# Kernel tuning notes

Measured on AMD Instinct MI355X. Metric: run time of the kernel, lower is better.

## Reference

```python
import jax, jax.numpy as jnp
import numpy as np

G = 32; N = G * G          # gridsize, num_nodes per graph
A = 16                      # n_agents
B = 32                      # batch_size
E = 4096                    # edges per graph (~4-neighbor grid)
F_IN = 16                   # input_dim
H = 64                      # hidden_dim
L = 3                       # n_graph_layers
MID = F_IN + L * H          # 208
CAT = 2 * MID + H           # 480
MIN_VAL = -1e8


def _layer_norm(x, g, b, eps=1e-5):
    m = x.mean(-1, keepdims=True)
    v = x.var(-1, keepdims=True)
    return (x - m) * jax.lax.rsqrt(v + eps) * g + b


def setup_inputs() -> dict:
    key = jax.random.key(0)
    ks = jax.random.split(key, 16)
    inp = {}
    inp["graph_nodes"] = jax.random.normal(ks[0], (B, N, F_IN), jnp.float32)
    inp["graph_edge_links"] = jax.random.randint(ks[1], (B, 2, E), 0, N)
    inp["agent_locations"] = jax.random.randint(ks[2], (B, A), 0, N)
    inp["mask"] = jax.random.bernoulli(ks[3], 0.5, (B, A * N))
    inp["dist_matrix"] = jax.random.uniform(ks[4], (N, N), jnp.float32)
    dims = [F_IN] + [H] * L
    k = 5
    for l in range(L):
        inp[f"conv{l}_W"] = jax.random.normal(ks[k], (dims[l], H), jnp.float32) * 0.05
        inp[f"conv{l}_b"] = jnp.zeros((H,), jnp.float32)
        inp[f"conv{l}_g"] = jnp.ones((H,), jnp.float32)
        inp[f"conv{l}_beta"] = jnp.zeros((H,), jnp.float32)
        k += 1
    inp["edges_W"] = jax.random.normal(ks[k], (1, H), jnp.float32) * 0.05
    inp["edges_b"] = jnp.zeros((H,), jnp.float32)
    inp["actor1_W"] = jax.random.normal(ks[k + 1], (CAT, MID), jnp.float32) * 0.05
    inp["actor1_b"] = jnp.zeros((MID,), jnp.float32)
    inp["bn_g"] = jnp.ones((MID,), jnp.float32)
    inp["bn_b"] = jnp.zeros((MID,), jnp.float32)
    inp["actor2_W"] = jax.random.normal(ks[k + 2], (MID, 1), jnp.float32) * 0.05
    inp["actor2_b"] = jnp.zeros((1,), jnp.float32)
    return inp


def reference(graph_nodes, graph_edge_links, agent_locations, mask, dist_matrix,
              conv0_W, conv0_b, conv0_g, conv0_beta,
              conv1_W, conv1_b, conv1_g, conv1_beta,
              conv2_W, conv2_b, conv2_g, conv2_beta,
              edges_W, edges_b, actor1_W, actor1_b, bn_g, bn_b,
              actor2_W, actor2_b):
    # --- batch graphs: offset node indices per graph (Batch.from_data_list) ---
    x = graph_nodes.reshape(B * N, F_IN)
    offs = (jnp.arange(B) * N)[:, None, None]
    ei = (graph_edge_links + offs).transpose(1, 0, 2).reshape(2, B * E)
    src, dst = ei[0], ei[1]

    conv_params = [(conv0_W, conv0_b, conv0_g, conv0_beta),
                   (conv1_W, conv1_b, conv1_g, conv1_beta),
                   (conv2_W, conv2_b, conv2_g, conv2_beta)]
    outs = [x]
    for W, bb, g, beta in conv_params:
        # GINConv with eps=-1: (1+eps)*x_i == 0, so out = mlp(sum_j x_j)
        agg = jax.ops.segment_sum(x[src], dst, num_segments=B * N)
        x = jax.nn.relu(_layer_norm(agg @ W + bb, g, beta))  # mlp relu; outer .relu() idempotent
        outs.append(x)
    xc = jnp.concatenate(outs, axis=1).reshape(B, N, MID)

    # --- all-pairs (agent, node) feature build ---
    a = jnp.take_along_axis(xc, agent_locations[:, :, None], axis=1)  # [B, A, MID]
    a = jnp.repeat(a, N, axis=1)                                      # [B, A*N, MID]
    bfeat = jnp.tile(xc, (1, A, 1))                                   # [B, A*N, MID]
    c = dist_matrix[agent_locations].reshape(B, A * N, 1)             # [B, A*N, 1]
    c = c @ edges_W + edges_b                                         # [B, A*N, H]
    h = jnp.concatenate([a, bfeat, c], axis=2).reshape(-1, CAT)

    h = h @ actor1_W + actor1_b
    mu = h.mean(0)
    var = h.var(0)
    h = (h - mu) * jax.lax.rsqrt(var + 1e-5) * bn_g + bn_b  # BatchNorm1d, training stats
    h = jax.nn.relu(h)
    logits = (h @ actor2_W + actor2_b).reshape(B, A * N)
    logits = jnp.where(mask, logits, MIN_VAL)
    return jax.nn.softmax(logits, axis=1)
```

## Files before the change

kernel.cpp:

```cpp
#include <hip/hip_runtime.h>
#include <cstddef>

#define B_    32
#define N_    1024
#define E_    4096
#define A_    16
#define FIN_  16
#define H_    64
#define MID_  208
#define NODES (B_ * N_)
#define NEDGE (B_ * E_)
#define ROWS  (B_ * A_ * N_)
#define AN_   (A_ * N_)

__device__ __forceinline__ float readlane_f(float v, int l) {
  return __uint_as_float(__builtin_amdgcn_readlane(__float_as_uint(v), l));
}

__global__ __launch_bounds__(256) void k_front(const int* __restrict__ el,
                                               const float* __restrict__ dist,
                                               const int* __restrict__ loc,
                                               const float* __restrict__ W1,
                                               const float* __restrict__ eW,
                                               const float* __restrict__ eb,
                                               const float* __restrict__ b1,
                                               int* __restrict__ rowptr,
                                               int* __restrict__ counts,
                                               int* __restrict__ ssrc,
                                               float* __restrict__ d1row,
                                               float* __restrict__ c2row,
                                               float* __restrict__ e1,
                                               float* __restrict__ cu,
                                               float* __restrict__ base) {
  __shared__ int cnt[1024];
  __shared__ int cur[1024];
  __shared__ int part[256];
  __shared__ int loc_s[16];
  int blk = blockIdx.x, t = threadIdx.x;
  if (blk < 32) {
    int b = blk;
    for (int i = t; i < 1024; i += 256) cnt[i] = 0;
    __syncthreads();
    const int* srcp = el + b * (2 * E_);
    const int* dstp = srcp + E_;
    for (int i = t; i < E_; i += 256) atomicAdd(&cnt[dstp[i]], 1);
    __syncthreads();
    int4 c4 = *(const int4*)&cnt[t * 4];
    int s = c4.x + c4.y + c4.z + c4.w;
    part[t] = s;
    __syncthreads();
    for (int off = 1; off < 256; off <<= 1) {
      int v = (t >= off) ? part[t - off] : 0;
      __syncthreads();
      part[t] += v;
      __syncthreads();
    }
    int prev = ((t == 0) ? 0 : part[t - 1]) + b * E_;
    int p0 = prev, p1 = p0 + c4.x, p2 = p1 + c4.y, p3 = p2 + c4.z;
    *(int4*)&rowptr[b * 1024 + t * 4] = make_int4(p0, p1, p2, p3);
    *(int4*)&counts[b * 1024 + t * 4] = c4;
    cur[t * 4 + 0] = p0;
    cur[t * 4 + 1] = p1;
    cur[t * 4 + 2] = p2;
    cur[t * 4 + 3] = p3;
    __syncthreads();
    for (int i = t; i < E_; i += 256) {
      int dl = dstp[i];
      int sl = srcp[i];
      int pos = atomicAdd(&cur[dl], 1);
      ssrc[pos] = b * N_ + sl;
    }
  } else if (blk < 288) {
    int lane = t & 63, w = t >> 6;
    int r = (blk - 32) * 4 + w;
    const float* dr = dist + (size_t)r * N_;
    float s = 0.f, c2 = 0.f;
#pragma unroll
    for (int k = 0; k < 16; k++) {
      float v = dr[lane + 64 * k];
      s += v;
      c2 = fmaf(v, v, c2);
    }
#pragma unroll
    for (int o = 32; o > 0; o >>= 1) { s += __shfl_xor(s, o); c2 += __shfl_xor(c2, o); }
    if (lane == 0) { d1row[r] = s; c2row[r] = c2; }
  } else if (blk < 320) {
    int b = blk - 288;
    if (t < 16) loc_s[t] = loc[b * 16 + t];
    __syncthreads();
    float e4[4] = {0.f, 0.f, 0.f, 0.f};
    for (int a = 0; a < 16; a++) {
      const float* dr = dist + (size_t)loc_s[a] * N_;
#pragma unroll
      for (int k = 0; k < 4; k++) e4[k] += dr[t + 256 * k];
    }
#pragma unroll
    for (int k = 0; k < 4; k++) e1[b * N_ + t + 256 * k] = e4[k];
  } else {
    int j = t;
    if (j < MID_) {
      float c = 0.f, bs = 0.f;
      for (int k = 0; k < H_; k++) {
        float w = W1[(2 * MID_ + k) * MID_ + j];
        c = fmaf(eW[k], w, c);
        bs = fmaf(eb[k], w, bs);
      }
      cu[j] = c;
      base[j] = bs + b1[j];
    }
  }
}

template <int FINT, bool COPYIN>
__global__ __launch_bounds__(256) void k_layer(const float* __restrict__ xin, int xstride, int in_off,
                                               float* __restrict__ xc, int out_off,
                                               const int* __restrict__ rowptr,
                                               const int* __restrict__ counts,
                                               const int* __restrict__ ssrc,
                                               const float* __restrict__ W,
                                               const float* __restrict__ bias,
                                               const float* __restrict__ g,
                                               const float* __restrict__ beta) {
  int t = threadIdx.x, lane = t & 63, w = t >> 6;
  float Wcol[FINT];
#pragma unroll
  for (int f = 0; f < FINT; f++) Wcol[f] = W[f * 64 + lane];
  float bv = bias[lane], gv = g[lane], bev = beta[lane];
  constexpr int CH = 64 / FINT;
  int f = lane & (FINT - 1);
  int ch = (FINT == 64) ? 0 : (lane >> 4);
  int nbase = (blockIdx.x * 4 + w) * 8;

  float agg[8];
#pragma unroll
  for (int nn = 0; nn < 8; nn++) {
    int node = nbase + nn;
    int r0 = rowptr[node];
    int deg = counts[node];
    float a0 = 0.f, a1 = 0.f, a2 = 0.f, a3 = 0.f;
    int e = ch;
    for (; e + 3 * CH < deg; e += 4 * CH) {
      int s0 = ssrc[r0 + e];
      int s1 = ssrc[r0 + e + CH];
      int s2 = ssrc[r0 + e + 2 * CH];
      int s3 = ssrc[r0 + e + 3 * CH];
      a0 += xin[(size_t)s0 * xstride + in_off + f];
      a1 += xin[(size_t)s1 * xstride + in_off + f];
      a2 += xin[(size_t)s2 * xstride + in_off + f];
      a3 += xin[(size_t)s3 * xstride + in_off + f];
    }
    for (; e < deg; e += CH) {
      int s = ssrc[r0 + e];
      a0 += xin[(size_t)s * xstride + in_off + f];
    }
    agg[nn] = (a0 + a1) + (a2 + a3);
  }

#pragma unroll
  for (int nn = 0; nn < 8; nn++) {
    int node = nbase + nn;
    float aggf = agg[nn];
    float y0 = bv, y1 = 0.f, y2 = 0.f, y3 = 0.f;
#pragma unroll
    for (int l = 0; l < 64; l += 4) {
      y0 = fmaf(readlane_f(aggf, l + 0), Wcol[(l + 0) & (FINT - 1)], y0);
      y1 = fmaf(readlane_f(aggf, l + 1), Wcol[(l + 1) & (FINT - 1)], y1);
      y2 = fmaf(readlane_f(aggf, l + 2), Wcol[(l + 2) & (FINT - 1)], y2);
      y3 = fmaf(readlane_f(aggf, l + 3), Wcol[(l + 3) & (FINT - 1)], y3);
    }
    float y = (y0 + y1) + (y2 + y3);
    float m = y;
#pragma unroll
    for (int o = 32; o > 0; o >>= 1) m += __shfl_xor(m, o);
    m *= (1.f / 64.f);
    float d = y - m;
    float vv = d * d;
#pragma unroll
    for (int o = 32; o > 0; o >>= 1) vv += __shfl_xor(vv, o);
    vv *= (1.f / 64.f);
    float outv = fmaxf(d * rsqrtf(vv + 1e-5f) * gv + bev, 0.f);
    xc[(size_t)node * MID_ + out_off + lane] = outv;
    if (COPYIN) {
      if (lane < FIN_) xc[(size_t)node * MID_ + lane] = xin[(size_t)node * FIN_ + lane];
    }
  }
}

template <int NR>
__device__ __forceinline__ void gemm_sc(const float* __restrict__ xc,
                                        const float* __restrict__ W1,
                                        int row0w, int j0, float acc[NR][4]) {
  const float* Bbase = W1 + (size_t)MID_ * MID_;
  const float* Arow = xc + (size_t)row0w * MID_;
#pragma unroll
  for (int r = 0; r < NR; r++)
#pragma unroll
    for (int q = 0; q < 4; q++) acc[r][q] = 0.f;

#pragma unroll 2
  for (int c = 0; c < 52; c++) {
    int k = c * 4;
    float4 a[NR];
    const float* ap = Arow + k;
#pragma unroll
    for (int r = 0; r < NR; r++) a[r] = *(const float4*)(ap + r * MID_);
#pragma unroll
    for (int q = 0; q < 4; q++) {
      float4 bq = *(const float4*)(Bbase + (size_t)(k + q) * MID_ + j0);
#pragma unroll
      for (int r = 0; r < NR; r++) {
        float ar = (q == 0) ? a[r].x : (q == 1) ? a[r].y : (q == 2) ? a[r].z : a[r].w;
        acc[r][0] = fmaf(ar, bq.x, acc[r][0]);
        acc[r][1] = fmaf(ar, bq.y, acc[r][1]);
        acc[r][2] = fmaf(ar, bq.z, acc[r][2]);
        acc[r][3] = fmaf(ar, bq.w, acc[r][3]);
      }
    }
  }
}

#define TSTR 105
__global__ __launch_bounds__(256) void k_p1(const float* __restrict__ xc,
                                            const float* __restrict__ W1,
                                            const float* __restrict__ e1,
                                            const int* __restrict__ loc,
                                            float* __restrict__ SBp,
                                            float* __restrict__ pBT,
                                            float* __restrict__ pA) {
  __shared__ float red[4 * 624];
  __shared__ float accS[32 * TSTR];
  __shared__ float xr[MID_];
  int t = threadIdx.x, lane = t & 63;
  int w = __builtin_amdgcn_readfirstlane(t >> 6);
  int blk = blockIdx.x;
  if (blk < 1024) {
    int row0 = blk * 32;
    int row0w = row0 + w * 8;
    int j0 = lane * 4;
    float acc[8][4];
    gemm_sc<8>(xc, W1, row0w, j0, acc);
    const float* ep = e1 + row0w;
    float4 e0 = *(const float4*)(ep);
    float4 e4 = *(const float4*)(ep + 4);
    float ev[8] = {e0.x, e0.y, e0.z, e0.w, e4.x, e4.y, e4.z, e4.w};
    if (j0 < MID_) {
      float s1[4] = {0, 0, 0, 0}, s2[4] = {0, 0, 0, 0}, se[4] = {0, 0, 0, 0};
#pragma unroll
      for (int r = 0; r < 8; r++) {
#pragma unroll
        for (int q = 0; q < 4; q++) {
          float v = acc[r][q];
          s1[q] += v;
          s2[q] = fmaf(v, v, s2[q]);
          se[q] = fmaf(v, ev[r], se[q]);
        }
      }
#pragma unroll
      for (int q = 0; q < 4; q++) {
        red[w * 624 + j0 + q] = s1[q];
        red[w * 624 + 208 + j0 + q] = s2[q];
        red[w * 624 + 416 + j0 + q] = se[q];
      }
    }
    __syncthreads();
    for (int idx = t; idx < 624; idx += 256) {
      SBp[(size_t)blk * 624 + idx] =
          (red[idx] + red[624 + idx]) + (red[1248 + idx] + red[1872 + idx]);
    }
#pragma unroll
    for (int half = 0; half < 2; half++) {
      int lo = half * 104;
      __syncthreads();
      if (j0 >= lo && j0 < lo + 104) {
        int jc = j0 - lo;
#pragma unroll
        for (int r = 0; r < 8; r++) {
          int ba = (w * 8 + r) * TSTR + jc;
          accS[ba + 0] = acc[r][0];
          accS[ba + 1] = acc[r][1];
          accS[ba + 2] = acc[r][2];
          accS[ba + 3] = acc[r][3];
        }
      }
      __syncthreads();
      int jb = lo + w * 26;
      if (lane < 32) {
#pragma unroll 2
        for (int jj = 0; jj < 26; jj++) {
          int j = jb + jj;
          pBT[(size_t)j * NODES + row0 + lane] = accS[lane * TSTR + (j - lo)];
        }
      }
    }
  } else {
    int ab = blk - 1024;
    int b = ab >> 4;
    int node = b * N_ + loc[ab];
    if (t < MID_) xr[t] = xc[(size_t)node * MID_ + t];
    __syncthreads();
    if (t < MID_) {
      float acc = 0.f;
      for (int i = 0; i < MID_; i++) acc = fmaf(xr[i], W1[i * MID_ + t], acc);
      pA[ab * MID_ + t] = acc;
    }
  }
}

__global__ __launch_bounds__(256) void k_fin(const float* __restrict__ SBp,
                                             const float* __restrict__ pA,
                                             const float* __restrict__ cu,
                                             const float* __restrict__ base,
                                             const float* __restrict__ d1row,
                                             const float* __restrict__ c2row,
                                             const int* __restrict__ loc,
                                             const float* __restrict__ bng,
                                             const float* __restrict__ bnb,
                                             const float* __restrict__ W2,
                                             float* __restrict__ vaT,
                                             float* __restrict__ wpack4) {
  __shared__ float utmp[1536 + 192];
  __shared__ float redm[4];
  __shared__ float reds[4];
  __shared__ float bcast[2];
  int t = threadIdx.x, lane = t & 63, w = t >> 6;
  int j = blockIdx.x;
  float cuj = cu[j], bj = base[j];
  int bb = t >> 3, ii = t & 7;
  float q1 = 0, q2 = 0, q3 = 0, t1 = 0, t2 = 0, t3 = 0;
#pragma unroll
  for (int i = ii * 4; i < ii * 4 + 4; i++) {
    const float* sp = SBp + (size_t)(bb * 32 + i) * 624;
    q1 += sp[j];
    q2 += sp[208 + j];
    q3 += sp[416 + j];
  }
#pragma unroll
  for (int a = ii * 2; a < ii * 2 + 2; a++) {
    int r = bb * 16 + a;
    float pa = pA[r * MID_ + j] + bj;
    t1 += pa;
    t2 = fmaf(pa, pa, t2);
    t3 = fmaf(pa, d1row[loc[r]], t3);
  }
  utmp[0 * 256 + t] = q1;
  utmp[1 * 256 + t] = q2;
  utmp[2 * 256 + t] = q3;
  utmp[3 * 256 + t] = t1;
  utmp[4 * 256 + t] = t2;
  utmp[5 * 256 + t] = t3;
  float p1 = 0.f, p2 = 0.f;
#pragma unroll
  for (int r = t * 2; r < t * 2 + 2; r++) {
    int l = loc[r];
    p1 += d1row[l];
    p2 += c2row[l];
  }
#pragma unroll
  for (int o = 32; o > 0; o >>= 1) { p1 += __shfl_xor(p1, o); p2 += __shfl_xor(p2, o); }
  if (lane == 0) { redm[w] = p1; reds[w] = p2; }
  __syncthreads();
  if (t < 192) {
    int s = t >> 5, b32 = t & 31;
    float ssum = 0.f;
#pragma unroll
    for (int i = 0; i < 8; i++) ssum += utmp[s * 256 + b32 * 8 + i];
    utmp[1536 + s * 32 + b32] = ssum;
  }
  __syncthreads();
  if (t == 0) {
    float Sc1 = (redm[0] + redm[1]) + (redm[2] + redm[3]);
    float Sc2 = (reds[0] + reds[1]) + (reds[2] + reds[3]);
    double T1 = 0, T2 = 0, T3 = 0, cross = 0, sp1 = 0, sp2 = 0, spe = 0;
    for (int b = 0; b < 32; b++) {
      float sq1 = utmp[1536 + 0 * 32 + b];
      float sq2 = utmp[1536 + 1 * 32 + b];
      float sq3 = utmp[1536 + 2 * 32 + b];
      float pt1 = utmp[1536 + 3 * 32 + b];
      float pt2 = utmp[1536 + 4 * 32 + b];
      float pt3 = utmp[1536 + 5 * 32 + b];
      T1 += pt1; T2 += pt2; T3 += pt3;
      cross += (double)pt1 * sq1;
      sp1 += sq1; sp2 += sq2; spe += sq3;
    }
    double s1 = 1024.0 * T1 + 16.0 * sp1 + (double)cuj * Sc1;
    double s2 = 1024.0 * T2 + 16.0 * sp2 + (double)cuj * cuj * Sc2 +
                2.0 * (cross + (double)cuj * (T3 + spe));
    double mu = s1 * (1.0 / (double)ROWS);
    double var = s2 * (1.0 / (double)ROWS) - mu * mu;
    float sc = (float)(1.0 / sqrt(var + 1e-5)) * bng[j];
    float sh = bnb[j] - (float)mu * sc;
    bcast[0] = sc;
    bcast[1] = sh;
    wpack4[4 * j + 0] = sc;
    wpack4[4 * j + 1] = cuj * sc;
    wpack4[4 * j + 2] = W2[j];
    wpack4[4 * j + 3] = 0.f;
  }
  __syncthreads();
  float sc = bcast[0], sh = bcast[1];
#pragma unroll
  for (int r = t * 2; r < t * 2 + 2; r++) {
    int b = r >> 4, a = r & 15;
    float pa = pA[r * MID_ + j] + bj;
    vaT[((size_t)b * MID_ + j) * 16 + a] = pa * sc + sh;
  }
}

__global__ __launch_bounds__(256) void k_logits(const float* __restrict__ pBT,
                                                const float* __restrict__ vaT,
                                                const float* __restrict__ wpack4,
                                                const float* __restrict__ dist,
                                                const int* __restrict__ loc,
                                                const int* __restrict__ mask,
                                                const float* __restrict__ b2,
                                                float* __restrict__ lg,
                                                float2* __restrict__ Psm) {
  __shared__ float accL[4][8][64];
  __shared__ int loc_s[16];
  __shared__ float redm[4];
  __shared__ float reds[4];
  int t = threadIdx.x, lane = t & 63;
  int w = __builtin_amdgcn_readfirstlane(t >> 6);
  int b = blockIdx.y, nt = blockIdx.x;
  int n0 = nt * 64;
  if (t < 16) loc_s[t] = loc[b * 16 + t];
  __syncthreads();
  float c[16];
#pragma unroll
  for (int a = 0; a < 16; a++) c[a] = dist[(size_t)loc_s[a] * N_ + n0 + lane];
  float acc16[16];
#pragma unroll
  for (int a = 0; a < 16; a++) acc16[a] = 0.f;
  const float4* wp = (const float4*)wpack4;
  int ng = b * N_ + n0 + lane;
  int jb = w * 52;
#pragma unroll 4
  for (int jj = 0; jj < 52; jj++) {
    int j = jb + jj;
    float pbv = pBT[(size_t)j * NODES + ng];
    float4 wv = wp[j];
    float pbs = pbv * wv.x;
    const float* va = vaT + ((size_t)b * MID_ + j) * 16;
#pragma unroll
    for (int a = 0; a < 16; a++) {
      float h = fmaf(c[a], wv.y, va[a] + pbs);
      h = fmaxf(h, 0.f);
      acc16[a] = fmaf(h, wv.z, acc16[a]);
    }
  }

  float b2v = b2[0];
  float sv[4];
  int ois[4];
  unsigned mk = 0;
#pragma unroll
  for (int half = 0; half < 2; half++) {
#pragma unroll
    for (int a8 = 0; a8 < 8; a8++) accL[t >> 6][a8][lane] = acc16[half * 8 + a8];
    __syncthreads();
#pragma unroll
    for (int p = 0; p < 2; p++) {
      int idx = p * 256 + t;
      int a8 = idx >> 6, nn = idx & 63;
      float s = (accL[0][a8][nn] + accL[1][a8][nn]) +
                (accL[2][a8][nn] + accL[3][a8][nn]) + b2v;
      int a = half * 8 + a8;
      int oi = b * AN_ + a * N_ + n0 + nn;
      int iv = half * 2 + p;
      bool m_ = mask[oi] != 0;
      sv[iv] = m_ ? s : -1e8f;
      ois[iv] = oi;
      mk |= (m_ ? 1u : 0u) << iv;
    }
    __syncthreads();
  }

  float mx = fmaxf(fmaxf(sv[0], sv[1]), fmaxf(sv[2], sv[3]));
#pragma unroll
  for (int o = 32; o > 0; o >>= 1) mx = fmaxf(mx, __shfl_xor(mx, o));
  if (lane == 0) redm[t >> 6] = mx;
  __syncthreads();
  mx = fmaxf(fmaxf(redm[0], redm[1]), fmaxf(redm[2], redm[3]));
  float ssum = 0.f;
#pragma unroll
  for (int iv = 0; iv < 4; iv++) {
    float pv = ((mk >> iv) & 1u) ? expf(sv[iv] - mx) : 0.f;
    lg[ois[iv]] = pv;
    ssum += pv;
  }
#pragma unroll
  for (int o = 32; o > 0; o >>= 1) ssum += __shfl_xor(ssum, o);
  if (lane == 0) reds[t >> 6] = ssum;
  __syncthreads();
  if (t == 0) Psm[b * 16 + nt] = make_float2(mx, (reds[0] + reds[1]) + (reds[2] + reds[3]));
}

__global__ __launch_bounds__(256) void k_sm2(const float* __restrict__ lg,
                                             const float2* __restrict__ P,
                                             float* __restrict__ out) {
  __shared__ float scs[16];
  int b = blockIdx.y, x = blockIdx.x, t = threadIdx.x;
  float M = -3.0e38f;
  float2 pr[16];
#pragma unroll
  for (int k = 0; k < 16; k++) {
    pr[k] = P[b * 16 + k];
    M = fmaxf(M, pr[k].x);
  }
  float S = 0.f;
#pragma unroll
  for (int k = 0; k < 16; k++) S += pr[k].y * expf(pr[k].x - M);
  float inv = 1.0f / S;
  if (t < 16) scs[t] = expf(pr[t].x - M) * inv;
  __syncthreads();
  const float* lb = lg + b * AN_ + x * 2048;
  float* ob = out + b * AN_ + x * 2048;
#pragma unroll
  for (int k = 0; k < 8; k++) {
    int i = t + 256 * k;
    int n = (x * 2048 + i) & 1023;
    ob[i] = lb[i] * scs[n >> 6];
  }
}

extern "C" void kernel_launch(void* const* d_in, const int* in_sizes, int n_in,
                              void* d_out, int out_size, void* d_ws, size_t ws_size,
                              hipStream_t stream) {
  const float* gn = (const float*)d_in[0];
  const int* el = (const int*)d_in[1];
  const int* loc = (const int*)d_in[2];
  const int* mask = (const int*)d_in[3];
  const float* dist = (const float*)d_in[4];
  const float* c0W = (const float*)d_in[5];
  const float* c0b = (const float*)d_in[6];
  const float* c0g = (const float*)d_in[7];
  const float* c0be = (const float*)d_in[8];
  const float* c1W = (const float*)d_in[9];
  const float* c1b = (const float*)d_in[10];
  const float* c1g = (const float*)d_in[11];
  const float* c1be = (const float*)d_in[12];
  const float* c2W = (const float*)d_in[13];
  const float* c2b = (const float*)d_in[14];
  const float* c2g = (const float*)d_in[15];
  const float* c2be = (const float*)d_in[16];
  const float* eW = (const float*)d_in[17];
  const float* eb = (const float*)d_in[18];
  const float* W1 = (const float*)d_in[19];
  const float* b1 = (const float*)d_in[20];
  const float* bng = (const float*)d_in[21];
  const float* bnb = (const float*)d_in[22];
  const float* W2 = (const float*)d_in[23];
  const float* b2 = (const float*)d_in[24];
  float* out = (float*)d_out;

  char* p = (char*)d_ws;
  auto alloc = [&](size_t bytes) {
    char* r = p;
    p += (bytes + 255) & ~(size_t)255;
    return r;
  };
  int* counts = (int*)alloc((size_t)NODES * 4);
  int* rowptr = (int*)alloc((size_t)NODES * 4);
  int* ssrc = (int*)alloc((size_t)NEDGE * 4);
  float* xc = (float*)alloc((size_t)NODES * MID_ * 4);
  float* pBT = (float*)alloc((size_t)NODES * MID_ * 4);
  float* pA = (float*)alloc((size_t)512 * MID_ * 4);
  float* cu = (float*)alloc(256 * 4);
  float* base = (float*)alloc(256 * 4);
  float* d1row = (float*)alloc((size_t)N_ * 4);
  float* c2row = (float*)alloc((size_t)N_ * 4);
  float* e1 = (float*)alloc((size_t)B_ * N_ * 4);
  float* SBp = (float*)alloc((size_t)1024 * 624 * 4);
  float* vaT = (float*)alloc((size_t)B_ * MID_ * 16 * 4);
  float* wpack4 = (float*)alloc((size_t)MID_ * 4 * 4);
  float* lg = (float*)alloc((size_t)ROWS * 4);
  float2* Psm = (float2*)alloc((size_t)B_ * 16 * 8);

  k_front<<<321, 256, 0, stream>>>(el, dist, loc, W1, eW, eb, b1,
                                   rowptr, counts, ssrc, d1row, c2row, e1, cu, base);

  k_layer<16, true><<<1024, 256, 0, stream>>>(gn, FIN_, 0, xc, 16, rowptr, counts, ssrc, c0W, c0b, c0g, c0be);
  k_layer<64, false><<<1024, 256, 0, stream>>>(xc, MID_, 16, xc, 80, rowptr, counts, ssrc, c1W, c1b, c1g, c1be);
  k_layer<64, false><<<1024, 256, 0, stream>>>(xc, MID_, 80, xc, 144, rowptr, counts, ssrc, c2W, c2b, c2g, c2be);

  k_p1<<<1536, 256, 0, stream>>>(xc, W1, e1, loc, SBp, pBT, pA);
  k_fin<<<208, 256, 0, stream>>>(SBp, pA, cu, base, d1row, c2row, loc, bng, bnb, W2, vaT, wpack4);

  k_logits<<<dim3(16, 32), 256, 0, stream>>>(pBT, vaT, wpack4, dist, loc, mask, b2, lg, Psm);
  k_sm2<<<dim3(8, 32), 256, 0, stream>>>(lg, Psm, out);
}
```

Measured before the change: 268.0 us.

## Fuse softmax normalization into logits kernel via last-block counter; stage vaT and ssrc in LDS

The separate softmax-rescale kernel is removed. Instead, the last block of each batch, found through an atomic counter, rescales all of that batch's logits. The per-batch vaT slice is loaded into shared memory so the inner loop reads from LDS rather than global memory. The CSR source indices are first scattered into LDS and then written out coalesced. This saves one launch and some scattered global traffic, but leaves a single block per batch to serialize the final 16K-element rescale pass.

Measured after the change: 333.4 us. +24.4%, slower.

```diff
diff --git a/kernel.cpp b/kernel.cpp
--- a/kernel.cpp
+++ b/kernel.cpp
@@ -31,10 +31,12 @@
                                                float* __restrict__ c2row,
                                                float* __restrict__ e1,
                                                float* __restrict__ cu,
-                                               float* __restrict__ base) {
+                                               float* __restrict__ base,
+                                               int* __restrict__ cnt32) {
   __shared__ int cnt[1024];
   __shared__ int cur[1024];
   __shared__ int part[256];
+  __shared__ int ssrcS[4096];
   __shared__ int loc_s[16];
   int blk = blockIdx.x, t = threadIdx.x;
   if (blk < 32) {
@@ -55,9 +57,9 @@
       part[t] += v;
       __syncthreads();
     }
-    int prev = ((t == 0) ? 0 : part[t - 1]) + b * E_;
+    int prev = (t == 0) ? 0 : part[t - 1];
     int p0 = prev, p1 = p0 + c4.x, p2 = p1 + c4.y, p3 = p2 + c4.z;
-    *(int4*)&rowptr[b * 1024 + t * 4] = make_int4(p0, p1, p2, p3);
+    *(int4*)&rowptr[b * 1024 + t * 4] = make_int4(p0 + b * E_, p1 + b * E_, p2 + b * E_, p3 + b * E_);
     *(int4*)&counts[b * 1024 + t * 4] = c4;
     cur[t * 4 + 0] = p0;
     cur[t * 4 + 1] = p1;
@@ -68,8 +70,10 @@
       int dl = dstp[i];
       int sl = srcp[i];
       int pos = atomicAdd(&cur[dl], 1);
-      ssrc[pos] = b * N_ + sl;
-    }
+      ssrcS[pos] = b * N_ + sl;
+    }
+    __syncthreads();
+    for (int i = t; i < E_; i += 256) ssrc[b * E_ + i] = ssrcS[i];
   } else if (blk < 288) {
     int lane = t & 63, w = t >> 6;
     int r = (blk - 32) * 4 + w;
@@ -98,6 +102,7 @@
     for (int k = 0; k < 4; k++) e1[b * N_ + t + 256 * k] = e4[k];
   } else {
     int j = t;
+    if (t < 32) cnt32[t] = 0;
     if (j < MID_) {
       float c = 0.f, bs = 0.f;
       for (int k = 0; k < H_; k++) {
@@ -414,16 +419,22 @@
                                                 const int* __restrict__ mask,
                                                 const float* __restrict__ b2,
                                                 float* __restrict__ lg,
-                                                float2* __restrict__ Psm) {
+                                                float2* __restrict__ Psm,
+                                                int* __restrict__ cnt32,
+                                                float* __restrict__ out) {
+  __shared__ float vaS[MID_ * 16];
   __shared__ float accL[4][8][64];
   __shared__ int loc_s[16];
   __shared__ float redm[4];
   __shared__ float reds[4];
+  __shared__ int lastFlag;
+  __shared__ float scs2[16];
   int t = threadIdx.x, lane = t & 63;
   int w = __builtin_amdgcn_readfirstlane(t >> 6);
   int b = blockIdx.y, nt = blockIdx.x;
   int n0 = nt * 64;
   if (t < 16) loc_s[t] = loc[b * 16 + t];
+  for (int i = t; i < MID_ * 16; i += 256) vaS[i] = vaT[(size_t)b * MID_ * 16 + i];
   __syncthreads();
   float c[16];
 #pragma unroll
@@ -440,7 +451,7 @@
     float pbv = pBT[(size_t)j * NODES + ng];
     float4 wv = wp[j];
     float pbs = pbv * wv.x;
-    const float* va = vaT + ((size_t)b * MID_ + j) * 16;
+    const float* va = &vaS[j * 16];
 #pragma unroll
     for (int a = 0; a < 16; a++) {
       float h = fmaf(c[a], wv.y, va[a] + pbs);
@@ -493,33 +504,34 @@
   if (lane == 0) reds[t >> 6] = ssum;
   __syncthreads();
   if (t == 0) Psm[b * 16 + nt] = make_float2(mx, (reds[0] + reds[1]) + (reds[2] + reds[3]));
-}
-
-__global__ __launch_bounds__(256) void k_sm2(const float* __restrict__ lg,
-                                             const float2* __restrict__ P,
-                                             float* __restrict__ out) {
-  __shared__ float scs[16];
-  int b = blockIdx.y, x = blockIdx.x, t = threadIdx.x;
+
+  __threadfence();
+  __syncthreads();
+  if (t == 0) {
+    int old = atomicAdd(&cnt32[b], 1);
+    lastFlag = (old == 15);
+  }
+  __syncthreads();
+  if (!lastFlag) return;
+  __threadfence();
   float M = -3.0e38f;
   float2 pr[16];
 #pragma unroll
   for (int k = 0; k < 16; k++) {
-    pr[k] = P[b * 16 + k];
+    pr[k] = Psm[b * 16 + k];
     M = fmaxf(M, pr[k].x);
   }
   float S = 0.f;
 #pragma unroll
   for (int k = 0; k < 16; k++) S += pr[k].y * expf(pr[k].x - M);
   float inv = 1.0f / S;
-  if (t < 16) scs[t] = expf(pr[t].x - M) * inv;
-  __syncthreads();
-  const float* lb = lg + b * AN_ + x * 2048;
-  float* ob = out + b * AN_ + x * 2048;
-#pragma unroll
-  for (int k = 0; k < 8; k++) {
-    int i = t + 256 * k;
-    int n = (x * 2048 + i) & 1023;
-    ob[i] = lb[i] * scs[n >> 6];
+  if (t < 16) scs2[t] = expf(pr[t].x - M) * inv;
+  __syncthreads();
+  const float* lb = lg + b * AN_;
+  float* ob = out + b * AN_;
+  for (int i = t; i < AN_; i += 256) {
+    int node = i & 1023;
+    ob[i] = lb[i] * scs2[node >> 6];
   }
 }
 
@@ -575,9 +587,10 @@
   float* wpack4 = (float*)alloc((size_t)MID_ * 4 * 4);
   float* lg = (float*)alloc((size_t)ROWS * 4);
   float2* Psm = (float2*)alloc((size_t)B_ * 16 * 8);
+  int* cnt32 = (int*)alloc(32 * 4);
 
   k_front<<<321, 256, 0, stream>>>(el, dist, loc, W1, eW, eb, b1,
-                                   rowptr, counts, ssrc, d1row, c2row, e1, cu, base);
+                                   rowptr, counts, ssrc, d1row, c2row, e1, cu, base, cnt32);
 
   k_layer<16, true><<<1024, 256, 0, stream>>>(gn, FIN_, 0, xc, 16, rowptr, counts, ssrc, c0W, c0b, c0g, c0be);
   k_layer<64, false><<<1024, 256, 0, stream>>>(xc, MID_, 16, xc, 80, rowptr, counts, ssrc, c1W, c1b, c1g, c1be);
@@ -586,6 +599,5 @@
   k_p1<<<1536, 256, 0, stream>>>(xc, W1, e1, loc, SBp, pBT, pA);
   k_fin<<<208, 256, 0, stream>>>(SBp, pA, cu, base, d1row, c2row, loc, bng, bnb, W2, vaT, wpack4);
 
-  k_logits<<<dim3(16, 32), 256, 0, stream>>>(pBT, vaT, wpack4, dist, loc, mask, b2, lg, Psm);
-  k_sm2<<<dim3(8, 32), 256, 0, stream>>>(lg, Psm, out);
-}
+  k_logits<<<dim3(16, 32), 256, 0, stream>>>(pBT, vaT, wpack4, dist, loc, mask, b2, lg, Psm, cnt32, out);
+}
```
